# Optimization experiments

Measured on AMD Instinct MI355X. Metric: run time of the kernel, lower is better.

The kernel has to match this reference:

```python
import jax, jax.numpy as jnp
import numpy as np

B, D, H1, H2, E, O = 32768, 256, 512, 256, 16, 64


def setup_inputs() -> dict:
    key = jax.random.key(0)
    ks = jax.random.split(key, 12)
    s = lambda fan_in: 1.0 / np.sqrt(fan_in)
    return {
        "x": jax.random.normal(ks[0], (B, D), dtype=jnp.float32),
        "gate_w": jax.random.normal(ks[1], (D, E), dtype=jnp.float32) * s(D),
        "gate_b": jnp.zeros((E,), dtype=jnp.float32),
        "W1": jax.random.normal(ks[2], (E, D, H1), dtype=jnp.float32) * s(D),
        "b1": jnp.zeros((E, H1), dtype=jnp.float32),
        "W2": jax.random.normal(ks[3], (E, H1, H2), dtype=jnp.float32) * s(H1),
        "b2": jnp.zeros((E, H2), dtype=jnp.float32),
        "W3": jax.random.normal(ks[4], (E, H2, O), dtype=jnp.float32) * s(H2),
        "b3": jnp.zeros((E, O), dtype=jnp.float32),
        "head_w": jax.random.normal(ks[5], (O, 1), dtype=jnp.float32) * s(O),
        "head_b": jnp.zeros((1,), dtype=jnp.float32),
    }


def reference(x, gate_w, gate_b, W1, b1, W2, b2, W3, b3, head_w, head_b):
    # gating: softmax over experts, [B, E]
    gates = jax.nn.softmax(x @ gate_w + gate_b, axis=-1)
    # all-expert dense MLP as batched GEMMs over leading expert axis
    h1 = jax.nn.relu(jnp.einsum('bd,edh->ebh', x, W1) + b1[:, None, :])   # [E,B,H1]
    h2 = jax.nn.relu(jnp.einsum('ebh,ehk->ebk', h1, W2) + b2[:, None, :])  # [E,B,H2]
    eo = jnp.einsum('ebk,eko->ebo', h2, W3) + b3[:, None, :]               # [E,B,O]
    # gated combination: sum_e gates[b,e] * eo[e,b,:]
    fused = jnp.einsum('be,ebo->bo', gates, eo)                            # [B,O]
    yts = (fused @ head_w + head_b)[:, 0]                                  # [B]
    return yts
```

## Files before the change

### kernel.cpp

```cpp
#include <hip/hip_runtime.h>

#define B_TOK 32768
#define D_IN  256
#define H1D   512
#define H2D   256
#define NE    16
#define NO    64

typedef _Float16 half8 __attribute__((ext_vector_type(8)));
typedef _Float16 half4 __attribute__((ext_vector_type(4)));
typedef float   float4_t __attribute__((ext_vector_type(4)));

__global__ void prep_kernel(const float* __restrict__ W1, const float* __restrict__ W2,
                            const float* __restrict__ W3, const float* __restrict__ b3,
                            const float* __restrict__ hw, const float* __restrict__ gw,
                            _Float16* __restrict__ w1p, _Float16* __restrict__ w2p,
                            float* __restrict__ w3h, float* __restrict__ c3,
                            _Float16* __restrict__ gwp) {
  int blk = blockIdx.x;
  int tid = threadIdx.x;
  if (blk < 1024) {
    int t = blk * 256 + tid;
    int lane = t & 63;
    int kt   = (t >> 6) & 7;
    int ntg  = (t >> 9) & 31;
    int e    = t >> 14;
    int n  = ntg * 16 + (lane & 15);
    int kb = kt * 32 + (lane >> 4) * 8;
    half8 v;
    #pragma unroll
    for (int j = 0; j < 8; ++j)
      v[j] = (_Float16)W1[((size_t)(e * D_IN + kb + j)) * H1D + n];
    *(half8*)(w1p + (size_t)t * 8) = v;
  } else if (blk < 2048) {
    int t = (blk - 1024) * 256 + tid;
    int lane = t & 63;
    int ktg  = (t >> 6) & 15;
    int ntg  = (t >> 10) & 15;
    int e    = t >> 14;
    int n  = ntg * 16 + (lane & 15);
    int kb = ktg * 32 + (lane >> 4) * 8;
    half8 v;
    #pragma unroll
    for (int j = 0; j < 8; ++j)
      v[j] = (_Float16)W2[((size_t)(e * H1D + kb + j)) * H2D + n];
    *(half8*)(w2p + (size_t)t * 8) = v;
  } else if (blk < 2065) {
    int t = (blk - 2048) * 256 + tid;
    if (t < NE * H2D) {
      int e = t >> 8, h = t & 255;
      float s = 0.f;
      #pragma unroll
      for (int o = 0; o < NO; ++o) s = fmaf(W3[((size_t)(e * H2D + h)) * NO + o], hw[o], s);
      w3h[t] = s;
    } else if (t < NE * H2D + NE) {
      int e = t - NE * H2D;
      float s = 0.f;
      #pragma unroll
      for (int o = 0; o < NO; ++o) s = fmaf(b3[e * NO + o], hw[o], s);
      c3[e] = s;
    }
  } else {
    for (int t = tid; t < 512; t += 256) {
      int lane = t & 63;
      int kt   = t >> 6;
      int e  = lane & 15;
      int kb = kt * 32 + (lane >> 4) * 8;
      half8 v;
      #pragma unroll
      for (int j = 0; j < 8; ++j)
        v[j] = (_Float16)gw[(kb + j) * NE + e];
      *(half8*)(gwp + (size_t)t * 8) = v;
    }
  }
}

#define H1CSTR 266

__global__ __launch_bounds__(256, 2) void moe_main(
    const float* __restrict__ x,
    const float* __restrict__ b1,
    const float* __restrict__ b2,
    const _Float16* __restrict__ w1p,
    const _Float16* __restrict__ w2p,
    const _Float16* __restrict__ gwp,
    const float* __restrict__ gb,
    const float* __restrict__ w3h,
    const float* __restrict__ c3,
    const float* __restrict__ head_b,
    float* __restrict__ out) {
  __shared__ _Float16 x_lds[32 * 512];
  __shared__ _Float16 h1c[64 * H1CSTR];
  __shared__ float g_lds[64 * 17];
  __shared__ float fin[4 * 64];

  const int tid  = threadIdx.x;
  const int w    = tid >> 6;
  const int lane = tid & 63;
  const int q    = lane >> 4;
  const int l16  = lane & 15;
  const int m0   = blockIdx.x * 64;

  #pragma unroll
  for (int f = 0; f < 8; ++f) {
    const float* xr = x + (size_t)(m0 + w * 16 + l16) * D_IN + f * 32 + q * 8;
    float4_t v0 = *(const float4_t*)(xr);
    float4_t v1 = *(const float4_t*)(xr + 4);
    half8 h;
    h[0] = (_Float16)v0[0]; h[1] = (_Float16)v0[1];
    h[2] = (_Float16)v0[2]; h[3] = (_Float16)v0[3];
    h[4] = (_Float16)v1[0]; h[5] = (_Float16)v1[1];
    h[6] = (_Float16)v1[2]; h[7] = (_Float16)v1[3];
    *(half8*)(x_lds + (size_t)(w * 8 + f) * 512 + lane * 8) = h;
  }
  __syncthreads();

  {
    float gbv = gb[l16];
    float4_t lg = (float4_t){0.f, 0.f, 0.f, 0.f};
    #pragma unroll
    for (int kt = 0; kt < 8; ++kt) {
      half8 xa = *(const half8*)(x_lds + (size_t)(w * 8 + kt) * 512 + lane * 8);
      half8 bfr = *(const half8*)(gwp + (size_t)kt * 512 + lane * 8);
      lg = __builtin_amdgcn_mfma_f32_16x16x32_f16(xa, bfr, lg, 0, 0, 0);
    }
    #pragma unroll
    for (int r = 0; r < 4; ++r) {
      float v = lg[r] + gbv;
      float m = v;
      m = fmaxf(m, __shfl_xor(m, 1));
      m = fmaxf(m, __shfl_xor(m, 2));
      m = fmaxf(m, __shfl_xor(m, 4));
      m = fmaxf(m, __shfl_xor(m, 8));
      float p = __expf(v - m);
      float s = p;
      s += __shfl_xor(s, 1);
      s += __shfl_xor(s, 2);
      s += __shfl_xor(s, 4);
      s += __shfl_xor(s, 8);
      g_lds[(w * 16 + q * 4 + r) * 17 + l16] = p / s;
    }
  }

  float yacc[4][4];
  #pragma unroll
  for (int mt = 0; mt < 4; ++mt)
    #pragma unroll
    for (int r = 0; r < 4; ++r) yacc[mt][r] = 0.f;

  for (int e = 0; e < NE; ++e) {
    float4_t h2[4][4];
    #pragma unroll
    for (int mt = 0; mt < 4; ++mt)
      #pragma unroll
      for (int nt = 0; nt < 4; ++nt)
        h2[mt][nt] = (float4_t){0.f, 0.f, 0.f, 0.f};

    #pragma unroll
    for (int ch = 0; ch < 2; ++ch) {
      float4_t a1[4][4];
      #pragma unroll
      for (int mt = 0; mt < 4; ++mt)
        #pragma unroll
        for (int nt = 0; nt < 4; ++nt)
          a1[mt][nt] = (float4_t){0.f, 0.f, 0.f, 0.f};

      const _Float16* w1e =
          w1p + ((size_t)((e * 32 + ch * 16 + w * 4) * 8)) * 512 + lane * 8;
      #pragma unroll
      for (int kt = 0; kt < 8; ++kt) {
        half8 wc[4];
        #pragma unroll
        for (int mt = 0; mt < 4; ++mt)
          wc[mt] = *(const half8*)(w1e + (size_t)(mt * 8 + kt) * 512);
        half8 xb[4];
        #pragma unroll
        for (int nt = 0; nt < 4; ++nt)
          xb[nt] = *(const half8*)(x_lds + (size_t)(nt * 8 + kt) * 512 + lane * 8);
        #pragma unroll
        for (int mt = 0; mt < 4; ++mt)
          #pragma unroll
          for (int nt = 0; nt < 4; ++nt)
            a1[mt][nt] = __builtin_amdgcn_mfma_f32_16x16x32_f16(
                wc[mt], xb[nt], a1[mt][nt], 0, 0, 0);
      }

      #pragma unroll
      for (int mt = 0; mt < 4; ++mt) {
        int colbase = (w * 4 + mt) * 16 + q * 4;
        float4_t bb = *(const float4_t*)(b1 + e * H1D + ch * 256 + colbase);
        #pragma unroll
        for (int nt = 0; nt < 4; ++nt) {
          half4 hv;
          #pragma unroll
          for (int r = 0; r < 4; ++r)
            hv[r] = (_Float16)fmaxf(a1[mt][nt][r] + bb[r], 0.f);
          *(half4*)(h1c + (nt * 16 + l16) * H1CSTR + colbase) = hv;
        }
      }

      __syncthreads();

      const _Float16* w2e =
          w2p + ((size_t)((e * 16 + w * 4) * 16 + ch * 8)) * 512 + lane * 8;
      #pragma unroll
      for (int kt = 0; kt < 8; ++kt) {
        half8 w2c[4];
        #pragma unroll
        for (int nt = 0; nt < 4; ++nt)
          w2c[nt] = *(const half8*)(w2e + (size_t)(nt * 16 + kt) * 512);
        half8 hac[4];
        #pragma unroll
        for (int mt = 0; mt < 4; ++mt)
          hac[mt] = *(const half8*)(h1c + (mt * 16 + l16) * H1CSTR + kt * 32 + q * 8);
        #pragma unroll
        for (int mt = 0; mt < 4; ++mt)
          #pragma unroll
          for (int nt = 0; nt < 4; ++nt)
            h2[mt][nt] = __builtin_amdgcn_mfma_f32_16x16x32_f16(
                hac[mt], w2c[nt], h2[mt][nt], 0, 0, 0);
      }

      __syncthreads();
    }

    float b2v[4], w3v[4];
    #pragma unroll
    for (int nt = 0; nt < 4; ++nt) {
      int n = w * 64 + nt * 16 + l16;
      b2v[nt] = b2[e * H2D + n];
      w3v[nt] = w3h[e * H2D + n];
    }
    #pragma unroll
    for (int mt = 0; mt < 4; ++mt) {
      #pragma unroll
      for (int r = 0; r < 4; ++r) {
        float s = 0.f;
        #pragma unroll
        for (int nt = 0; nt < 4; ++nt)
          s += fmaxf(h2[mt][nt][r] + b2v[nt], 0.f) * w3v[nt];
        yacc[mt][r] += g_lds[(mt * 16 + q * 4 + r) * 17 + e] * s;
      }
    }
  }

  #pragma unroll
  for (int mt = 0; mt < 4; ++mt) {
    #pragma unroll
    for (int r = 0; r < 4; ++r) {
      float v = yacc[mt][r];
      v += __shfl_xor(v, 1);
      v += __shfl_xor(v, 2);
      v += __shfl_xor(v, 4);
      v += __shfl_xor(v, 8);
      yacc[mt][r] = v;
    }
  }
  if (l16 == 0) {
    #pragma unroll
    for (int mt = 0; mt < 4; ++mt)
      #pragma unroll
      for (int r = 0; r < 4; ++r)
        fin[w * 64 + mt * 16 + q * 4 + r] = yacc[mt][r];
  }
  __syncthreads();
  if (tid < 64) {
    float sum = fin[tid] + fin[64 + tid] + fin[128 + tid] + fin[192 + tid];
    float gc = 0.f;
    #pragma unroll
    for (int e = 0; e < NE; ++e) gc += g_lds[tid * 17 + e] * c3[e];
    out[m0 + tid] = sum + gc + head_b[0];
  }
}

extern "C" void kernel_launch(void* const* d_in, const int* in_sizes, int n_in,
                              void* d_out, int out_size, void* d_ws, size_t ws_size,
                              hipStream_t stream) {
  const float* x      = (const float*)d_in[0];
  const float* gate_w = (const float*)d_in[1];
  const float* gate_b = (const float*)d_in[2];
  const float* W1     = (const float*)d_in[3];
  const float* b1     = (const float*)d_in[4];
  const float* W2     = (const float*)d_in[5];
  const float* b2     = (const float*)d_in[6];
  const float* W3     = (const float*)d_in[7];
  const float* b3     = (const float*)d_in[8];
  const float* head_w = (const float*)d_in[9];
  const float* head_b = (const float*)d_in[10];
  float* out = (float*)d_out;

  char* ws = (char*)d_ws;
  _Float16* w1p = (_Float16*)(ws);
  _Float16* w2p = (_Float16*)(ws + 4194304);
  _Float16* gwp = (_Float16*)(ws + 8388608);
  float*    w3h = (float*)(ws + 8396800);
  float*    c3  = (float*)(ws + 8413184);

  hipLaunchKernelGGL(prep_kernel, dim3(2066), dim3(256), 0, stream,
                     W1, W2, W3, b3, head_w, gate_w, w1p, w2p, w3h, c3, gwp);
  hipLaunchKernelGGL(moe_main, dim3(B_TOK / 64), dim3(256), 0, stream,
                     x, b1, b2, w1p, w2p, gwp, gate_b, w3h, c3, head_b, out);
}
```

Before: 363.9 us.

## Double-buffer H1 chunks and interleave layer-1 and layer-2 MFMA sweeps

Splits each expert's H1 activation into four 128-column chunks held in two alternating LDS buffers. Each warp computes tiles belonging to two chunks per sweep, so the store of one chunk and the layer-2 GEMM on the previous chunk can run between barriers. The goal is to cut barrier stalls and let layer-2 MFMAs overlap layer-1 epilogue work. In exchange the schedule is more intricate, a sync is added before the final chunk, and buffer reuse across experts now relies on the barrier ordering being correct.

```diff
diff --git a/kernel.cpp b/kernel.cpp
--- a/kernel.cpp
+++ b/kernel.cpp
@@ -75,7 +75,7 @@
   }
 }
 
-#define H1CSTR 266
+#define H1CSTR 136
 
 __global__ __launch_bounds__(256, 2) void moe_main(
     const float* __restrict__ x,
@@ -90,7 +90,7 @@
     const float* __restrict__ head_b,
     float* __restrict__ out) {
   __shared__ _Float16 x_lds[32 * 512];
-  __shared__ _Float16 h1c[64 * H1CSTR];
+  __shared__ _Float16 h1c[2][64 * H1CSTR];
   __shared__ float g_lds[64 * 17];
   __shared__ float fin[4 * 64];
 
@@ -156,55 +156,60 @@
       for (int nt = 0; nt < 4; ++nt)
         h2[mt][nt] = (float4_t){0.f, 0.f, 0.f, 0.f};
 
-    #pragma unroll
-    for (int ch = 0; ch < 2; ++ch) {
-      float4_t a1[4][4];
-      #pragma unroll
-      for (int mt = 0; mt < 4; ++mt)
+    float4_t a1[4][4];
+
+    auto sweep = [&](int s) {
+      #pragma unroll
+      for (int j = 0; j < 4; ++j)
         #pragma unroll
         for (int nt = 0; nt < 4; ++nt)
-          a1[mt][nt] = (float4_t){0.f, 0.f, 0.f, 0.f};
-
-      const _Float16* w1e =
-          w1p + ((size_t)((e * 32 + ch * 16 + w * 4) * 8)) * 512 + lane * 8;
+          a1[j][nt] = (float4_t){0.f, 0.f, 0.f, 0.f};
+      int tb = s * 16 + w * 2;
+      const _Float16* w1e = w1p + (size_t)(e * 32 * 8) * 512 + lane * 8;
       #pragma unroll
       for (int kt = 0; kt < 8; ++kt) {
-        half8 wc[4];
-        #pragma unroll
-        for (int mt = 0; mt < 4; ++mt)
-          wc[mt] = *(const half8*)(w1e + (size_t)(mt * 8 + kt) * 512);
-        half8 xb[4];
+        half8 wv[4];
+        wv[0] = *(const half8*)(w1e + (size_t)((tb + 0) * 8 + kt) * 512);
+        wv[1] = *(const half8*)(w1e + (size_t)((tb + 1) * 8 + kt) * 512);
+        wv[2] = *(const half8*)(w1e + (size_t)((tb + 8) * 8 + kt) * 512);
+        wv[3] = *(const half8*)(w1e + (size_t)((tb + 9) * 8 + kt) * 512);
+        half8 xv[4];
         #pragma unroll
         for (int nt = 0; nt < 4; ++nt)
-          xb[nt] = *(const half8*)(x_lds + (size_t)(nt * 8 + kt) * 512 + lane * 8);
-        #pragma unroll
-        for (int mt = 0; mt < 4; ++mt)
+          xv[nt] = *(const half8*)(x_lds + (size_t)(nt * 8 + kt) * 512 + lane * 8);
+        #pragma unroll
+        for (int j = 0; j < 4; ++j)
           #pragma unroll
           for (int nt = 0; nt < 4; ++nt)
-            a1[mt][nt] = __builtin_amdgcn_mfma_f32_16x16x32_f16(
-                wc[mt], xb[nt], a1[mt][nt], 0, 0, 0);
+            a1[j][nt] = __builtin_amdgcn_mfma_f32_16x16x32_f16(
+                wv[j], xv[nt], a1[j][nt], 0, 0, 0);
       }
-
-      #pragma unroll
-      for (int mt = 0; mt < 4; ++mt) {
-        int colbase = (w * 4 + mt) * 16 + q * 4;
-        float4_t bb = *(const float4_t*)(b1 + e * H1D + ch * 256 + colbase);
+    };
+
+    auto storechunk = [&](int c, int j0) {
+      _Float16* buf = h1c[c & 1];
+      #pragma unroll
+      for (int i = 0; i < 2; ++i) {
+        int lt = w * 2 + i;
+        int colbase = lt * 16 + q * 4;
+        float4_t bb = *(const float4_t*)(b1 + e * H1D + c * 128 + colbase);
         #pragma unroll
         for (int nt = 0; nt < 4; ++nt) {
           half4 hv;
           #pragma unroll
           for (int r = 0; r < 4; ++r)
-            hv[r] = (_Float16)fmaxf(a1[mt][nt][r] + bb[r], 0.f);
-          *(half4*)(h1c + (nt * 16 + l16) * H1CSTR + colbase) = hv;
+            hv[r] = (_Float16)fmaxf(a1[j0 + i][nt][r] + bb[r], 0.f);
+          *(half4*)(buf + (nt * 16 + l16) * H1CSTR + colbase) = hv;
         }
       }
-
-      __syncthreads();
-
+    };
+
+    auto l2chunk = [&](int c) {
+      const _Float16* buf = h1c[c & 1];
       const _Float16* w2e =
-          w2p + ((size_t)((e * 16 + w * 4) * 16 + ch * 8)) * 512 + lane * 8;
-      #pragma unroll
-      for (int kt = 0; kt < 8; ++kt) {
+          w2p + (size_t)((e * 16 + w * 4) * 16 + c * 4) * 512 + lane * 8;
+      #pragma unroll
+      for (int kt = 0; kt < 4; ++kt) {
         half8 w2c[4];
         #pragma unroll
         for (int nt = 0; nt < 4; ++nt)
@@ -212,7 +217,7 @@
         half8 hac[4];
         #pragma unroll
         for (int mt = 0; mt < 4; ++mt)
-          hac[mt] = *(const half8*)(h1c + (mt * 16 + l16) * H1CSTR + kt * 32 + q * 8);
+          hac[mt] = *(const half8*)(buf + (mt * 16 + l16) * H1CSTR + kt * 32 + q * 8);
         #pragma unroll
         for (int mt = 0; mt < 4; ++mt)
           #pragma unroll
@@ -220,9 +225,20 @@
             h2[mt][nt] = __builtin_amdgcn_mfma_f32_16x16x32_f16(
                 hac[mt], w2c[nt], h2[mt][nt], 0, 0, 0);
       }
-
-      __syncthreads();
-    }
+    };
+
+    sweep(0);
+    storechunk(0, 0);
+    __syncthreads();
+    storechunk(1, 2);
+    l2chunk(0);
+    __syncthreads();
+    l2chunk(1);
+    sweep(1);
+    storechunk(2, 0);
+    __syncthreads();
+    storechunk(3, 2);
+    l2chunk(2);
 
     float b2v[4], w3v[4];
     #pragma unroll
@@ -231,6 +247,9 @@
       b2v[nt] = b2[e * H2D + n];
       w3v[nt] = w3h[e * H2D + n];
     }
+    __syncthreads();
+    l2chunk(3);
+
     #pragma unroll
     for (int mt = 0; mt < 4; ++mt) {
       #pragma unroll
```

Result: slower. 453.7 us (+24.7%).
